# Kernel optimization log

Hardware: AMD Instinct MI355X
Metric: run time of the kernel (lower is better)

## Reference

```python
import jax, jax.numpy as jnp
import numpy as np

BLOCK_SIZE = 64
WINDOW_SIZE = 256  # local_window pattern: each query block attends to blocks within the window
NEG_INF = -1e30


def setup_inputs() -> dict:
    key = jax.random.key(0)
    kq, kk, kv = jax.random.split(key, 3)
    B, S, H, D = 2, 4096, 16, 64
    q = jax.random.normal(kq, (B, S, H, D), dtype=jnp.float32)
    k = jax.random.normal(kk, (B, S, H, D), dtype=jnp.float32)
    v = jax.random.normal(kv, (B, S, H, D), dtype=jnp.float32)
    return {"q": q, "k": k, "v": v}


def _block_sparse_attn(q, k, v):
    # q, k, v: [B, S, H, D]
    B, S, H, D = q.shape
    bs = BLOCK_SIZE
    N = S // bs                      # number of blocks
    W = WINDOW_SIZE // bs            # window in blocks (4)
    half = W // 2
    offsets = jnp.arange(-half, half + 1)          # [K] neighbor offsets, K = W+1 = 5
    K = offsets.shape[0]

    i = jnp.arange(N)
    j = i[:, None] + offsets[None, :]              # [N, K] neighbor block ids
    valid = (j >= 0) & (j < N)                     # boundary mask
    jc = jnp.clip(j, 0, N - 1)

    # reshape into blocks: [B, H, N, bs, D]
    qb = q.reshape(B, N, bs, H, D).transpose(0, 3, 1, 2, 4)
    kb = k.reshape(B, N, bs, H, D).transpose(0, 3, 1, 2, 4)
    vb = v.reshape(B, N, bs, H, D).transpose(0, 3, 1, 2, 4)

    # gather only the active (neighbor) key/value blocks: [B, H, N, K, bs, D]
    kn = kb[:, :, jc]
    vn = vb[:, :, jc]

    scale = 1.0 / jnp.sqrt(jnp.asarray(D, dtype=q.dtype))
    # block scores: [B, H, N, bs, K, bs]
    scores = jnp.einsum('bhnqd,bhnkcd->bhnqkc', qb, kn) * scale
    scores = jnp.where(valid[None, None, :, None, :, None], scores, NEG_INF)

    # softmax over the union of active key blocks for each query block
    scores = scores.reshape(B, H, N, bs, K * bs)
    attn = jax.nn.softmax(scores, axis=-1)
    out = jnp.einsum('bhnqe,bhned->bhnqd', attn, vn.reshape(B, H, N, K * bs, D))

    # back to [B, S, H, D]
    return out.transpose(0, 2, 3, 1, 4).reshape(B, S, H, D)


def reference(q, k, v):
    return _block_sparse_attn(q, k, v)
```

## Files before the change

### kernel.cpp

```cpp
#include <hip/hip_runtime.h>

#define S_DIM 4096
#define H_DIM 16
#define D_DIM 64
#define N_BLK 64
#define PITCH 72
#define NEG_INF_F (-1e30f)
#define QSCALE 0.125f

typedef __attribute__((ext_vector_type(4))) float f32x4;
typedef __attribute__((ext_vector_type(8))) short s16x8;
typedef __attribute__((ext_vector_type(4))) short s16x4;
typedef __attribute__((ext_vector_type(4))) unsigned int u32x4;
typedef __attribute__((ext_vector_type(2))) unsigned int u32x2;

__device__ __forceinline__ unsigned int fbits(float f) {
    return __builtin_bit_cast(unsigned int, f);
}
__device__ __forceinline__ unsigned int pkbf(float a, float b) {
    return __builtin_amdgcn_perm(fbits(b) + 0x8000u, fbits(a) + 0x8000u, 0x07060302u);
}
__device__ __forceinline__ short f2bf1(float f) {
    return (short)((fbits(f) + 0x8000u) >> 16);
}

__global__ __launch_bounds__(256, 4) void bsattn_kernel(
    const float* __restrict__ qg, const float* __restrict__ kg,
    const float* __restrict__ vg, float* __restrict__ outg)
{
    __shared__ short lds_k [N_BLK * PITCH];
    __shared__ short lds_vt[D_DIM * PITCH];

    const int tid  = threadIdx.x;
    const int w    = tid >> 6;
    const int lane = tid & 63;
    const int quad = lane >> 4;
    const int l16  = lane & 15;

    const int b  = blockIdx.z;
    const int h  = blockIdx.y;
    const int n0 = blockIdx.x << 1;
    const int n  = n0 + (w >> 1);
    const int qrow0 = n * 64 + (w & 1) * 32;

    s16x8 bq[2][2];
#pragma unroll
    for (int qt = 0; qt < 2; ++qt) {
        const size_t qrow = ((size_t)(b * S_DIM + qrow0 + qt * 16 + l16) * H_DIM + h) * D_DIM;
#pragma unroll
        for (int hh = 0; hh < 2; ++hh) {
            const float4* qp = reinterpret_cast<const float4*>(qg + qrow + hh * 32 + quad * 8);
            float4 f0 = qp[0];
            float4 f1 = qp[1];
            u32x4 u;
            u.x = pkbf(f0.x * QSCALE, f0.y * QSCALE);
            u.y = pkbf(f0.z * QSCALE, f0.w * QSCALE);
            u.z = pkbf(f1.x * QSCALE, f1.y * QSCALE);
            u.w = pkbf(f1.z * QSCALE, f1.w * QSCALE);
            bq[qt][hh] = __builtin_bit_cast(s16x8, u);
        }
    }

    f32x4 o[2][4];
    float m_run[2], l_run[2];
#pragma unroll
    for (int qt = 0; qt < 2; ++qt) {
        m_run[qt] = NEG_INF_F; l_run[qt] = 0.f;
#pragma unroll
        for (int dt = 0; dt < 4; ++dt) o[qt][dt] = (f32x4){0.f, 0.f, 0.f, 0.f};
    }

    const int tr = tid >> 2;
    const int d0 = (tid & 3) << 4;

    for (int ji = 0; ji < 6; ++ji) {
        const int j = n0 - 2 + ji;
        __syncthreads();
        if (j >= 0 && j < N_BLK) {
            const size_t src = ((size_t)(b * S_DIM + j * 64 + tr) * H_DIM + h) * D_DIM + d0;
            const float4* kp = reinterpret_cast<const float4*>(kg + src);
            const float4* vp = reinterpret_cast<const float4*>(vg + src);
            float4 k0 = kp[0], k1 = kp[1], k2 = kp[2], k3 = kp[3];
            float4 v0 = vp[0], v1 = vp[1], v2 = vp[2], v3 = vp[3];
            short* kd = lds_k + tr * PITCH + d0;
            u32x2 ka = {pkbf(k0.x, k0.y), pkbf(k0.z, k0.w)};
            u32x2 kb = {pkbf(k1.x, k1.y), pkbf(k1.z, k1.w)};
            u32x2 kc = {pkbf(k2.x, k2.y), pkbf(k2.z, k2.w)};
            u32x2 ke = {pkbf(k3.x, k3.y), pkbf(k3.z, k3.w)};
            *reinterpret_cast<u32x2*>(kd)      = ka;
            *reinterpret_cast<u32x2*>(kd + 4)  = kb;
            *reinterpret_cast<u32x2*>(kd + 8)  = kc;
            *reinterpret_cast<u32x2*>(kd + 12) = ke;
            float vf[16] = {v0.x, v0.y, v0.z, v0.w, v1.x, v1.y, v1.z, v1.w,
                            v2.x, v2.y, v2.z, v2.w, v3.x, v3.y, v3.z, v3.w};
#pragma unroll
            for (int i = 0; i < 16; ++i)
                lds_vt[(d0 + i) * PITCH + tr] = f2bf1(vf[i]);
        }
        __syncthreads();

        if (j < 0 || j >= N_BLK) continue;
        const int rel = j - n;
        if (rel < -2 || rel > 2) continue;

        f32x4 sa[2][4];
#pragma unroll
        for (int kt = 0; kt < 4; ++kt) {
            const short* kbp = lds_k + (kt * 16 + l16) * PITCH + quad * 8;
            s16x8 kf0 = *reinterpret_cast<const s16x8*>(kbp);
            s16x8 kf1 = *reinterpret_cast<const s16x8*>(kbp + 32);
            f32x4 z = {0.f, 0.f, 0.f, 0.f};
            f32x4 a0 = __builtin_amdgcn_mfma_f32_16x16x32_bf16(kf0, bq[0][0], z, 0, 0, 0);
            sa[0][kt] = __builtin_amdgcn_mfma_f32_16x16x32_bf16(kf1, bq[0][1], a0, 0, 0, 0);
            f32x4 a1 = __builtin_amdgcn_mfma_f32_16x16x32_bf16(kf0, bq[1][0], z, 0, 0, 0);
            sa[1][kt] = __builtin_amdgcn_mfma_f32_16x16x32_bf16(kf1, bq[1][1], a1, 0, 0, 0);
        }

        s16x8 pa[2][2];
#pragma unroll
        for (int qt = 0; qt < 2; ++qt) {
            float mx = NEG_INF_F;
#pragma unroll
            for (int kt = 0; kt < 4; ++kt)
#pragma unroll
                for (int r = 0; r < 4; ++r) mx = fmaxf(mx, sa[qt][kt][r]);
            mx = fmaxf(mx, __shfl_xor(mx, 16));
            mx = fmaxf(mx, __shfl_xor(mx, 32));
            const float mn = fmaxf(m_run[qt], mx);
            const float alpha = __expf(m_run[qt] - mn);
            m_run[qt] = mn;

            float rs = 0.f;
            unsigned int pk[4][2];
#pragma unroll
            for (int kt = 0; kt < 4; ++kt) {
                float e0 = __expf(sa[qt][kt][0] - mn);
                float e1 = __expf(sa[qt][kt][1] - mn);
                float e2 = __expf(sa[qt][kt][2] - mn);
                float e3 = __expf(sa[qt][kt][3] - mn);
                rs += (e0 + e1) + (e2 + e3);
                pk[kt][0] = pkbf(e0, e1);
                pk[kt][1] = pkbf(e2, e3);
            }
            rs += __shfl_xor(rs, 16);
            rs += __shfl_xor(rs, 32);
            l_run[qt] = l_run[qt] * alpha + rs;

            float ab[4];
#pragma unroll
            for (int r = 0; r < 4; ++r)
                ab[r] = __shfl(alpha, (lane & 48) + quad * 4 + r);
#pragma unroll
            for (int dt = 0; dt < 4; ++dt)
#pragma unroll
                for (int r = 0; r < 4; ++r) o[qt][dt][r] *= ab[r];

            pa[qt][0] = __builtin_bit_cast(s16x8, (u32x4){pk[0][0], pk[0][1], pk[1][0], pk[1][1]});
            pa[qt][1] = __builtin_bit_cast(s16x8, (u32x4){pk[2][0], pk[2][1], pk[3][0], pk[3][1]});
        }

#pragma unroll
        for (int dt = 0; dt < 4; ++dt) {
            const short* vb = lds_vt + (dt * 16 + l16) * PITCH + quad * 4;
            s16x4 v00 = *reinterpret_cast<const s16x4*>(vb);
            s16x4 v01 = *reinterpret_cast<const s16x4*>(vb + 16);
            s16x4 v10 = *reinterpret_cast<const s16x4*>(vb + 32);
            s16x4 v11 = *reinterpret_cast<const s16x4*>(vb + 48);
            s16x8 vf0 = {v00[0], v00[1], v00[2], v00[3], v01[0], v01[1], v01[2], v01[3]};
            s16x8 vf1 = {v10[0], v10[1], v10[2], v10[3], v11[0], v11[1], v11[2], v11[3]};
#pragma unroll
            for (int qt = 0; qt < 2; ++qt) {
                o[qt][dt] = __builtin_amdgcn_mfma_f32_16x16x32_bf16(pa[qt][0], vf0, o[qt][dt], 0, 0, 0);
                o[qt][dt] = __builtin_amdgcn_mfma_f32_16x16x32_bf16(pa[qt][1], vf1, o[qt][dt], 0, 0, 0);
            }
        }
    }

#pragma unroll
    for (int qt = 0; qt < 2; ++qt) {
#pragma unroll
        for (int r = 0; r < 4; ++r) {
            const float lb = __shfl(l_run[qt], (lane & 48) + quad * 4 + r);
            const float inv = 1.0f / lb;
            const int row = qrow0 + qt * 16 + quad * 4 + r;
            float* op = outg + ((size_t)(b * S_DIM + row) * H_DIM + h) * D_DIM + l16;
#pragma unroll
            for (int dt = 0; dt < 4; ++dt)
                op[dt * 16] = o[qt][dt][r] * inv;
        }
    }
}

extern "C" void kernel_launch(void* const* d_in, const int* in_sizes, int n_in,
                              void* d_out, int out_size, void* d_ws, size_t ws_size,
                              hipStream_t stream) {
    const float* q = (const float*)d_in[0];
    const float* k = (const float*)d_in[1];
    const float* v = (const float*)d_in[2];
    float* out = (float*)d_out;
    const int B = in_sizes[0] / (S_DIM * H_DIM * D_DIM);
    dim3 grid(N_BLK / 2, H_DIM, B);
    dim3 block(256);
    hipLaunchKernelGGL(bsattn_kernel, grid, block, 0, stream, q, k, v, out);
}
```

Baseline: 161.8 us.

## Double-buffer K/V tiles in LDS and prefetch next block into registers

Splits the K and transposed-V shared-memory tiles into two alternating buffers and issues the global loads for the next key block into registers before computing on the current one. This removes one barrier per iteration and lets global memory latency overlap with the MFMA and softmax work. In exchange it doubles LDS use (about 36 KB per block) and adds 32 live prefetch registers, which may reduce occupancy under the 4-blocks-per-CU launch bound.

After: 202.3 us. +25.0%, slower.

```diff
diff --git a/kernel.cpp b/kernel.cpp
--- a/kernel.cpp
+++ b/kernel.cpp
@@ -28,8 +28,8 @@
     const float* __restrict__ qg, const float* __restrict__ kg,
     const float* __restrict__ vg, float* __restrict__ outg)
 {
-    __shared__ short lds_k [N_BLK * PITCH];
-    __shared__ short lds_vt[D_DIM * PITCH];
+    __shared__ short lds_k [2 * N_BLK * PITCH];
+    __shared__ short lds_vt[2 * D_DIM * PITCH];
 
     const int tid  = threadIdx.x;
     const int w    = tid >> 6;
@@ -42,6 +42,22 @@
     const int n0 = blockIdx.x << 1;
     const int n  = n0 + (w >> 1);
     const int qrow0 = n * 64 + (w & 1) * 32;
+
+    const int tr = tid >> 2;
+    const int d0 = (tid & 3) << 4;
+    const size_t rowbase = ((size_t)(b * S_DIM + tr) * H_DIM + h) * D_DIM + d0;
+    const size_t jstride = (size_t)64 * H_DIM * D_DIM;
+
+    float4 pkf[4], pvf[4];
+    {
+        const int jn = n0 - 2;
+        if (jn >= 0) {
+            const float4* kp = reinterpret_cast<const float4*>(kg + rowbase + (size_t)jn * jstride);
+            const float4* vp = reinterpret_cast<const float4*>(vg + rowbase + (size_t)jn * jstride);
+            pkf[0] = kp[0]; pkf[1] = kp[1]; pkf[2] = kp[2]; pkf[3] = kp[3];
+            pvf[0] = vp[0]; pvf[1] = vp[1]; pvf[2] = vp[2]; pvf[3] = vp[3];
+        }
+    }
 
     s16x8 bq[2][2];
 #pragma unroll
@@ -70,108 +86,114 @@
         for (int dt = 0; dt < 4; ++dt) o[qt][dt] = (f32x4){0.f, 0.f, 0.f, 0.f};
     }
 
-    const int tr = tid >> 2;
-    const int d0 = (tid & 3) << 4;
-
     for (int ji = 0; ji < 6; ++ji) {
         const int j = n0 - 2 + ji;
-        __syncthreads();
+        const int bo = (ji & 1) * (N_BLK * PITCH);
+        short* const kbuf  = lds_k  + bo;
+        short* const vtbuf = lds_vt + bo;
+
         if (j >= 0 && j < N_BLK) {
-            const size_t src = ((size_t)(b * S_DIM + j * 64 + tr) * H_DIM + h) * D_DIM + d0;
-            const float4* kp = reinterpret_cast<const float4*>(kg + src);
-            const float4* vp = reinterpret_cast<const float4*>(vg + src);
-            float4 k0 = kp[0], k1 = kp[1], k2 = kp[2], k3 = kp[3];
-            float4 v0 = vp[0], v1 = vp[1], v2 = vp[2], v3 = vp[3];
-            short* kd = lds_k + tr * PITCH + d0;
-            u32x2 ka = {pkbf(k0.x, k0.y), pkbf(k0.z, k0.w)};
-            u32x2 kb = {pkbf(k1.x, k1.y), pkbf(k1.z, k1.w)};
-            u32x2 kc = {pkbf(k2.x, k2.y), pkbf(k2.z, k2.w)};
-            u32x2 ke = {pkbf(k3.x, k3.y), pkbf(k3.z, k3.w)};
+            short* kd = kbuf + tr * PITCH + d0;
+            u32x2 ka = {pkbf(pkf[0].x, pkf[0].y), pkbf(pkf[0].z, pkf[0].w)};
+            u32x2 kb = {pkbf(pkf[1].x, pkf[1].y), pkbf(pkf[1].z, pkf[1].w)};
+            u32x2 kc = {pkbf(pkf[2].x, pkf[2].y), pkbf(pkf[2].z, pkf[2].w)};
+            u32x2 ke = {pkbf(pkf[3].x, pkf[3].y), pkbf(pkf[3].z, pkf[3].w)};
             *reinterpret_cast<u32x2*>(kd)      = ka;
             *reinterpret_cast<u32x2*>(kd + 4)  = kb;
             *reinterpret_cast<u32x2*>(kd + 8)  = kc;
             *reinterpret_cast<u32x2*>(kd + 12) = ke;
-            float vf[16] = {v0.x, v0.y, v0.z, v0.w, v1.x, v1.y, v1.z, v1.w,
-                            v2.x, v2.y, v2.z, v2.w, v3.x, v3.y, v3.z, v3.w};
+            float vf[16] = {pvf[0].x, pvf[0].y, pvf[0].z, pvf[0].w,
+                            pvf[1].x, pvf[1].y, pvf[1].z, pvf[1].w,
+                            pvf[2].x, pvf[2].y, pvf[2].z, pvf[2].w,
+                            pvf[3].x, pvf[3].y, pvf[3].z, pvf[3].w};
 #pragma unroll
             for (int i = 0; i < 16; ++i)
-                lds_vt[(d0 + i) * PITCH + tr] = f2bf1(vf[i]);
+                vtbuf[(d0 + i) * PITCH + tr] = f2bf1(vf[i]);
         }
         __syncthreads();
 
-        if (j < 0 || j >= N_BLK) continue;
+        if (ji < 5) {
+            const int jn = j + 1;
+            if (jn >= 0 && jn < N_BLK) {
+                const float4* kp = reinterpret_cast<const float4*>(kg + rowbase + (size_t)jn * jstride);
+                const float4* vp = reinterpret_cast<const float4*>(vg + rowbase + (size_t)jn * jstride);
+                pkf[0] = kp[0]; pkf[1] = kp[1]; pkf[2] = kp[2]; pkf[3] = kp[3];
+                pvf[0] = vp[0]; pvf[1] = vp[1]; pvf[2] = vp[2]; pvf[3] = vp[3];
+            }
+        }
+
         const int rel = j - n;
-        if (rel < -2 || rel > 2) continue;
-
-        f32x4 sa[2][4];
-#pragma unroll
-        for (int kt = 0; kt < 4; ++kt) {
-            const short* kbp = lds_k + (kt * 16 + l16) * PITCH + quad * 8;
-            s16x8 kf0 = *reinterpret_cast<const s16x8*>(kbp);
-            s16x8 kf1 = *reinterpret_cast<const s16x8*>(kbp + 32);
-            f32x4 z = {0.f, 0.f, 0.f, 0.f};
-            f32x4 a0 = __builtin_amdgcn_mfma_f32_16x16x32_bf16(kf0, bq[0][0], z, 0, 0, 0);
-            sa[0][kt] = __builtin_amdgcn_mfma_f32_16x16x32_bf16(kf1, bq[0][1], a0, 0, 0, 0);
-            f32x4 a1 = __builtin_amdgcn_mfma_f32_16x16x32_bf16(kf0, bq[1][0], z, 0, 0, 0);
-            sa[1][kt] = __builtin_amdgcn_mfma_f32_16x16x32_bf16(kf1, bq[1][1], a1, 0, 0, 0);
-        }
-
-        s16x8 pa[2][2];
-#pragma unroll
-        for (int qt = 0; qt < 2; ++qt) {
-            float mx = NEG_INF_F;
-#pragma unroll
-            for (int kt = 0; kt < 4; ++kt)
-#pragma unroll
-                for (int r = 0; r < 4; ++r) mx = fmaxf(mx, sa[qt][kt][r]);
-            mx = fmaxf(mx, __shfl_xor(mx, 16));
-            mx = fmaxf(mx, __shfl_xor(mx, 32));
-            const float mn = fmaxf(m_run[qt], mx);
-            const float alpha = __expf(m_run[qt] - mn);
-            m_run[qt] = mn;
-
-            float rs = 0.f;
-            unsigned int pk[4][2];
+        if (j >= 0 && j < N_BLK && rel >= -2 && rel <= 2) {
+            f32x4 sa[2][4];
 #pragma unroll
             for (int kt = 0; kt < 4; ++kt) {
-                float e0 = __expf(sa[qt][kt][0] - mn);
-                float e1 = __expf(sa[qt][kt][1] - mn);
-                float e2 = __expf(sa[qt][kt][2] - mn);
-                float e3 = __expf(sa[qt][kt][3] - mn);
-                rs += (e0 + e1) + (e2 + e3);
-                pk[kt][0] = pkbf(e0, e1);
-                pk[kt][1] = pkbf(e2, e3);
-            }
-            rs += __shfl_xor(rs, 16);
-            rs += __shfl_xor(rs, 32);
-            l_run[qt] = l_run[qt] * alpha + rs;
-
-            float ab[4];
-#pragma unroll
-            for (int r = 0; r < 4; ++r)
-                ab[r] = __shfl(alpha, (lane & 48) + quad * 4 + r);
-#pragma unroll
-            for (int dt = 0; dt < 4; ++dt)
-#pragma unroll
-                for (int r = 0; r < 4; ++r) o[qt][dt][r] *= ab[r];
-
-            pa[qt][0] = __builtin_bit_cast(s16x8, (u32x4){pk[0][0], pk[0][1], pk[1][0], pk[1][1]});
-            pa[qt][1] = __builtin_bit_cast(s16x8, (u32x4){pk[2][0], pk[2][1], pk[3][0], pk[3][1]});
-        }
-
-#pragma unroll
-        for (int dt = 0; dt < 4; ++dt) {
-            const short* vb = lds_vt + (dt * 16 + l16) * PITCH + quad * 4;
-            s16x4 v00 = *reinterpret_cast<const s16x4*>(vb);
-            s16x4 v01 = *reinterpret_cast<const s16x4*>(vb + 16);
-            s16x4 v10 = *reinterpret_cast<const s16x4*>(vb + 32);
-            s16x4 v11 = *reinterpret_cast<const s16x4*>(vb + 48);
-            s16x8 vf0 = {v00[0], v00[1], v00[2], v00[3], v01[0], v01[1], v01[2], v01[3]};
-            s16x8 vf1 = {v10[0], v10[1], v10[2], v10[3], v11[0], v11[1], v11[2], v11[3]};
+                const short* kbp = kbuf + (kt * 16 + l16) * PITCH + quad * 8;
+                s16x8 kf0 = *reinterpret_cast<const s16x8*>(kbp);
+                s16x8 kf1 = *reinterpret_cast<const s16x8*>(kbp + 32);
+                f32x4 z = {0.f, 0.f, 0.f, 0.f};
+                f32x4 a0 = __builtin_amdgcn_mfma_f32_16x16x32_bf16(kf0, bq[0][0], z, 0, 0, 0);
+                sa[0][kt] = __builtin_amdgcn_mfma_f32_16x16x32_bf16(kf1, bq[0][1], a0, 0, 0, 0);
+                f32x4 a1 = __builtin_amdgcn_mfma_f32_16x16x32_bf16(kf0, bq[1][0], z, 0, 0, 0);
+                sa[1][kt] = __builtin_amdgcn_mfma_f32_16x16x32_bf16(kf1, bq[1][1], a1, 0, 0, 0);
+            }
+
+            s16x8 pa[2][2];
 #pragma unroll
             for (int qt = 0; qt < 2; ++qt) {
-                o[qt][dt] = __builtin_amdgcn_mfma_f32_16x16x32_bf16(pa[qt][0], vf0, o[qt][dt], 0, 0, 0);
-                o[qt][dt] = __builtin_amdgcn_mfma_f32_16x16x32_bf16(pa[qt][1], vf1, o[qt][dt], 0, 0, 0);
+                float mx = NEG_INF_F;
+#pragma unroll
+                for (int kt = 0; kt < 4; ++kt)
+#pragma unroll
+                    for (int r = 0; r < 4; ++r) mx = fmaxf(mx, sa[qt][kt][r]);
+                mx = fmaxf(mx, __shfl_xor(mx, 16));
+                mx = fmaxf(mx, __shfl_xor(mx, 32));
+                const float mn = fmaxf(m_run[qt], mx);
+                const float alpha = __expf(m_run[qt] - mn);
+                m_run[qt] = mn;
+
+                float rs = 0.f;
+                unsigned int pk[4][2];
+#pragma unroll
+                for (int kt = 0; kt < 4; ++kt) {
+                    float e0 = __expf(sa[qt][kt][0] - mn);
+                    float e1 = __expf(sa[qt][kt][1] - mn);
+                    float e2 = __expf(sa[qt][kt][2] - mn);
+                    float e3 = __expf(sa[qt][kt][3] - mn);
+                    rs += (e0 + e1) + (e2 + e3);
+                    pk[kt][0] = pkbf(e0, e1);
+                    pk[kt][1] = pkbf(e2, e3);
+                }
+                rs += __shfl_xor(rs, 16);
+                rs += __shfl_xor(rs, 32);
+                l_run[qt] = l_run[qt] * alpha + rs;
+
+                float ab[4];
+#pragma unroll
+                for (int r = 0; r < 4; ++r)
+                    ab[r] = __shfl(alpha, (lane & 48) + quad * 4 + r);
+#pragma unroll
+                for (int dt = 0; dt < 4; ++dt)
+#pragma unroll
+                    for (int r = 0; r < 4; ++r) o[qt][dt][r] *= ab[r];
+
+                pa[qt][0] = __builtin_bit_cast(s16x8, (u32x4){pk[0][0], pk[0][1], pk[1][0], pk[1][1]});
+                pa[qt][1] = __builtin_bit_cast(s16x8, (u32x4){pk[2][0], pk[2][1], pk[3][0], pk[3][1]});
+            }
+
+#pragma unroll
+            for (int dt = 0; dt < 4; ++dt) {
+                const short* vb = vtbuf + (dt * 16 + l16) * PITCH + quad * 4;
+                s16x4 v00 = *reinterpret_cast<const s16x4*>(vb);
+                s16x4 v01 = *reinterpret_cast<const s16x4*>(vb + 16);
+                s16x4 v10 = *reinterpret_cast<const s16x4*>(vb + 32);
+                s16x4 v11 = *reinterpret_cast<const s16x4*>(vb + 48);
+                s16x8 vf0 = {v00[0], v00[1], v00[2], v00[3], v01[0], v01[1], v01[2], v01[3]};
+                s16x8 vf1 = {v10[0], v10[1], v10[2], v10[3], v11[0], v11[1], v11[2], v11[3]};
+#pragma unroll
+                for (int qt = 0; qt < 2; ++qt) {
+                    o[qt][dt] = __builtin_amdgcn_mfma_f32_16x16x32_bf16(pa[qt][0], vf0, o[qt][dt], 0, 0, 0);
+                    o[qt][dt] = __builtin_amdgcn_mfma_f32_16x16x32_bf16(pa[qt][1], vf1, o[qt][dt], 0, 0, 0);
+                }
             }
         }
     }
```

## Give each wave a full query block, stage all V once, read K from global

Applied to the files above, without the earlier changes.

Each workgroup now covers four query blocks, one per wave. The union of eight V blocks is loaded into LDS once, transposed into packed bf16 pairs with a rotating swizzle, and followed by a single barrier. K fragments are loaded directly from global memory into registers per wave, which removes the per-iteration K staging and the pair of barriers per key block. The grid halves and the register footprint grows (launch bounds drop to 2 waves per SIMD). K reads are duplicated across waves and rely on cache, and LDS use grows to 64KB.

Result: no change. 160.6 us (-0.8%).

```diff
diff --git a/kernel.cpp b/kernel.cpp
--- a/kernel.cpp
+++ b/kernel.cpp
@@ -4,13 +4,11 @@
 #define H_DIM 16
 #define D_DIM 64
 #define N_BLK 64
-#define PITCH 72
 #define NEG_INF_F (-1e30f)
 #define QSCALE 0.125f
 
 typedef __attribute__((ext_vector_type(4))) float f32x4;
 typedef __attribute__((ext_vector_type(8))) short s16x8;
-typedef __attribute__((ext_vector_type(4))) short s16x4;
 typedef __attribute__((ext_vector_type(4))) unsigned int u32x4;
 typedef __attribute__((ext_vector_type(2))) unsigned int u32x2;
 
@@ -20,16 +18,12 @@
 __device__ __forceinline__ unsigned int pkbf(float a, float b) {
     return __builtin_amdgcn_perm(fbits(b) + 0x8000u, fbits(a) + 0x8000u, 0x07060302u);
 }
-__device__ __forceinline__ short f2bf1(float f) {
-    return (short)((fbits(f) + 0x8000u) >> 16);
-}
-
-__global__ __launch_bounds__(256, 4) void bsattn_kernel(
+
+__global__ __launch_bounds__(256, 2) void bsattn_kernel(
     const float* __restrict__ qg, const float* __restrict__ kg,
     const float* __restrict__ vg, float* __restrict__ outg)
 {
-    __shared__ short lds_k [N_BLK * PITCH];
-    __shared__ short lds_vt[D_DIM * PITCH];
+    __shared__ unsigned int lds_vt[D_DIM * 256];
 
     const int tid  = threadIdx.x;
     const int w    = tid >> 6;
@@ -39,14 +33,13 @@
 
     const int b  = blockIdx.z;
     const int h  = blockIdx.y;
-    const int n0 = blockIdx.x << 1;
-    const int n  = n0 + (w >> 1);
-    const int qrow0 = n * 64 + (w & 1) * 32;
-
-    s16x8 bq[2][2];
-#pragma unroll
-    for (int qt = 0; qt < 2; ++qt) {
-        const size_t qrow = ((size_t)(b * S_DIM + qrow0 + qt * 16 + l16) * H_DIM + h) * D_DIM;
+    const int n0 = blockIdx.x << 2;
+    const int n  = n0 + w;
+
+    s16x8 bq[4][2];
+#pragma unroll
+    for (int qt = 0; qt < 4; ++qt) {
+        const size_t qrow = ((size_t)(b * S_DIM + n * 64 + qt * 16 + l16) * H_DIM + h) * D_DIM;
 #pragma unroll
         for (int hh = 0; hh < 2; ++hh) {
             const float4* qp = reinterpret_cast<const float4*>(qg + qrow + hh * 32 + quad * 8);
@@ -61,69 +54,91 @@
         }
     }
 
-    f32x4 o[2][4];
-    float m_run[2], l_run[2];
-#pragma unroll
-    for (int qt = 0; qt < 2; ++qt) {
+    {
+        const int jt = tid >> 5;
+        const int sp = tid & 31;
+        const int jv = n0 - 2 + jt;
+        if (jv >= 0 && jv < N_BLK) {
+            const float* v0p = vg + ((size_t)(b * S_DIM + jv * 64 + 2 * sp) * H_DIM + h) * D_DIM;
+            const float* v1p = v0p + H_DIM * D_DIM;
+            const int craw = jt * 64 + 2 * sp;
+#pragma unroll
+            for (int ch = 0; ch < 4; ++ch) {
+                const int d0 = ch * 16;
+                const float4* ap = reinterpret_cast<const float4*>(v0p + d0);
+                const float4* bp = reinterpret_cast<const float4*>(v1p + d0);
+                float4 a0 = ap[0], a1 = ap[1], a2 = ap[2], a3 = ap[3];
+                float4 b0 = bp[0], b1 = bp[1], b2 = bp[2], b3 = bp[3];
+                float av[16] = {a0.x,a0.y,a0.z,a0.w, a1.x,a1.y,a1.z,a1.w,
+                                a2.x,a2.y,a2.z,a2.w, a3.x,a3.y,a3.z,a3.w};
+                float bv[16] = {b0.x,b0.y,b0.z,b0.w, b1.x,b1.y,b1.z,b1.w,
+                                b2.x,b2.y,b2.z,b2.w, b3.x,b3.y,b3.z,b3.w};
+#pragma unroll
+                for (int i = 0; i < 16; ++i) {
+                    const int d = d0 + i;
+                    lds_vt[d * 256 + (((craw + 8 * d) & 511) >> 1)] = pkbf(av[i], bv[i]);
+                }
+            }
+        }
+    }
+
+    f32x4 o[4][4];
+    float m_run[4], l_run[4];
+#pragma unroll
+    for (int qt = 0; qt < 4; ++qt) {
         m_run[qt] = NEG_INF_F; l_run[qt] = 0.f;
 #pragma unroll
         for (int dt = 0; dt < 4; ++dt) o[qt][dt] = (f32x4){0.f, 0.f, 0.f, 0.f};
     }
 
-    const int tr = tid >> 2;
-    const int d0 = (tid & 3) << 4;
-
-    for (int ji = 0; ji < 6; ++ji) {
-        const int j = n0 - 2 + ji;
-        __syncthreads();
-        if (j >= 0 && j < N_BLK) {
-            const size_t src = ((size_t)(b * S_DIM + j * 64 + tr) * H_DIM + h) * D_DIM + d0;
-            const float4* kp = reinterpret_cast<const float4*>(kg + src);
-            const float4* vp = reinterpret_cast<const float4*>(vg + src);
-            float4 k0 = kp[0], k1 = kp[1], k2 = kp[2], k3 = kp[3];
-            float4 v0 = vp[0], v1 = vp[1], v2 = vp[2], v3 = vp[3];
-            short* kd = lds_k + tr * PITCH + d0;
-            u32x2 ka = {pkbf(k0.x, k0.y), pkbf(k0.z, k0.w)};
-            u32x2 kb = {pkbf(k1.x, k1.y), pkbf(k1.z, k1.w)};
-            u32x2 kc = {pkbf(k2.x, k2.y), pkbf(k2.z, k2.w)};
-            u32x2 ke = {pkbf(k3.x, k3.y), pkbf(k3.z, k3.w)};
-            *reinterpret_cast<u32x2*>(kd)      = ka;
-            *reinterpret_cast<u32x2*>(kd + 4)  = kb;
-            *reinterpret_cast<u32x2*>(kd + 8)  = kc;
-            *reinterpret_cast<u32x2*>(kd + 12) = ke;
-            float vf[16] = {v0.x, v0.y, v0.z, v0.w, v1.x, v1.y, v1.z, v1.w,
-                            v2.x, v2.y, v2.z, v2.w, v3.x, v3.y, v3.z, v3.w};
-#pragma unroll
-            for (int i = 0; i < 16; ++i)
-                lds_vt[(d0 + i) * PITCH + tr] = f2bf1(vf[i]);
-        }
-        __syncthreads();
-
+    __syncthreads();
+
+    const int colb = quad * 4 + 8 * l16;
+
+    for (int t = 0; t < 5; ++t) {
+        const int j = n - 2 + t;
         if (j < 0 || j >= N_BLK) continue;
-        const int rel = j - n;
-        if (rel < -2 || rel > 2) continue;
-
-        f32x4 sa[2][4];
+        const int ji = w + t;
+
+        float4 kf[4][2][2];
 #pragma unroll
         for (int kt = 0; kt < 4; ++kt) {
-            const short* kbp = lds_k + (kt * 16 + l16) * PITCH + quad * 8;
-            s16x8 kf0 = *reinterpret_cast<const s16x8*>(kbp);
-            s16x8 kf1 = *reinterpret_cast<const s16x8*>(kbp + 32);
-            f32x4 z = {0.f, 0.f, 0.f, 0.f};
-            f32x4 a0 = __builtin_amdgcn_mfma_f32_16x16x32_bf16(kf0, bq[0][0], z, 0, 0, 0);
-            sa[0][kt] = __builtin_amdgcn_mfma_f32_16x16x32_bf16(kf1, bq[0][1], a0, 0, 0, 0);
-            f32x4 a1 = __builtin_amdgcn_mfma_f32_16x16x32_bf16(kf0, bq[1][0], z, 0, 0, 0);
-            sa[1][kt] = __builtin_amdgcn_mfma_f32_16x16x32_bf16(kf1, bq[1][1], a1, 0, 0, 0);
-        }
-
-        s16x8 pa[2][2];
-#pragma unroll
-        for (int qt = 0; qt < 2; ++qt) {
+            const size_t krow = ((size_t)(b * S_DIM + j * 64 + kt * 16 + l16) * H_DIM + h) * D_DIM + quad * 8;
+#pragma unroll
+            for (int hh = 0; hh < 2; ++hh) {
+                const float4* kp = reinterpret_cast<const float4*>(kg + krow + hh * 32);
+                kf[kt][hh][0] = kp[0];
+                kf[kt][hh][1] = kp[1];
+            }
+        }
+        s16x8 kbf[4][2];
+#pragma unroll
+        for (int kt = 0; kt < 4; ++kt)
+#pragma unroll
+            for (int hh = 0; hh < 2; ++hh) {
+                u32x4 u;
+                u.x = pkbf(kf[kt][hh][0].x, kf[kt][hh][0].y);
+                u.y = pkbf(kf[kt][hh][0].z, kf[kt][hh][0].w);
+                u.z = pkbf(kf[kt][hh][1].x, kf[kt][hh][1].y);
+                u.w = pkbf(kf[kt][hh][1].z, kf[kt][hh][1].w);
+                kbf[kt][hh] = __builtin_bit_cast(s16x8, u);
+            }
+
+        s16x8 pa[4][2];
+#pragma unroll
+        for (int qt = 0; qt < 4; ++qt) {
+            f32x4 sa[4];
+#pragma unroll
+            for (int kt = 0; kt < 4; ++kt) {
+                f32x4 z = {0.f, 0.f, 0.f, 0.f};
+                f32x4 a0 = __builtin_amdgcn_mfma_f32_16x16x32_bf16(kbf[kt][0], bq[qt][0], z, 0, 0, 0);
+                sa[kt]   = __builtin_amdgcn_mfma_f32_16x16x32_bf16(kbf[kt][1], bq[qt][1], a0, 0, 0, 0);
+            }
             float mx = NEG_INF_F;
 #pragma unroll
             for (int kt = 0; kt < 4; ++kt)
 #pragma unroll
-                for (int r = 0; r < 4; ++r) mx = fmaxf(mx, sa[qt][kt][r]);
+                for (int r = 0; r < 4; ++r) mx = fmaxf(mx, sa[kt][r]);
             mx = fmaxf(mx, __shfl_xor(mx, 16));
             mx = fmaxf(mx, __shfl_xor(mx, 32));
             const float mn = fmaxf(m_run[qt], mx);
@@ -134,10 +149,10 @@
             unsigned int pk[4][2];
 #pragma unroll
             for (int kt = 0; kt < 4; ++kt) {
-                float e0 = __expf(sa[qt][kt][0] - mn);
-                float e1 = __expf(sa[qt][kt][1] - mn);
-                float e2 = __expf(sa[qt][kt][2] - mn);
-                float e3 = __expf(sa[qt][kt][3] - mn);
+                float e0 = __expf(sa[kt][0] - mn);
+                float e1 = __expf(sa[kt][1] - mn);
+                float e2 = __expf(sa[kt][2] - mn);
+                float e3 = __expf(sa[kt][3] - mn);
                 rs += (e0 + e1) + (e2 + e3);
                 pk[kt][0] = pkbf(e0, e1);
                 pk[kt][1] = pkbf(e2, e3);
@@ -159,17 +174,20 @@
             pa[qt][1] = __builtin_bit_cast(s16x8, (u32x4){pk[2][0], pk[2][1], pk[3][0], pk[3][1]});
         }
 
+        const int cb0 = ji * 64 + colb;
 #pragma unroll
         for (int dt = 0; dt < 4; ++dt) {
-            const short* vb = lds_vt + (dt * 16 + l16) * PITCH + quad * 4;
-            s16x4 v00 = *reinterpret_cast<const s16x4*>(vb);
-            s16x4 v01 = *reinterpret_cast<const s16x4*>(vb + 16);
-            s16x4 v10 = *reinterpret_cast<const s16x4*>(vb + 32);
-            s16x4 v11 = *reinterpret_cast<const s16x4*>(vb + 48);
-            s16x8 vf0 = {v00[0], v00[1], v00[2], v00[3], v01[0], v01[1], v01[2], v01[3]};
-            s16x8 vf1 = {v10[0], v10[1], v10[2], v10[3], v11[0], v11[1], v11[2], v11[3]};
-#pragma unroll
-            for (int qt = 0; qt < 2; ++qt) {
+            const int d = dt * 16 + l16;
+            const unsigned int* vrow = lds_vt + d * 256;
+            const int cb = cb0 + 128 * dt;
+            u32x2 v00 = *reinterpret_cast<const u32x2*>(vrow + (((cb     ) & 511) >> 1));
+            u32x2 v01 = *reinterpret_cast<const u32x2*>(vrow + (((cb + 16) & 511) >> 1));
+            u32x2 v10 = *reinterpret_cast<const u32x2*>(vrow + (((cb + 32) & 511) >> 1));
+            u32x2 v11 = *reinterpret_cast<const u32x2*>(vrow + (((cb + 48) & 511) >> 1));
+            s16x8 vf0 = __builtin_bit_cast(s16x8, (u32x4){v00.x, v00.y, v01.x, v01.y});
+            s16x8 vf1 = __builtin_bit_cast(s16x8, (u32x4){v10.x, v10.y, v11.x, v11.y});
+#pragma unroll
+            for (int qt = 0; qt < 4; ++qt) {
                 o[qt][dt] = __builtin_amdgcn_mfma_f32_16x16x32_bf16(pa[qt][0], vf0, o[qt][dt], 0, 0, 0);
                 o[qt][dt] = __builtin_amdgcn_mfma_f32_16x16x32_bf16(pa[qt][1], vf1, o[qt][dt], 0, 0, 0);
             }
@@ -177,12 +195,12 @@
     }
 
 #pragma unroll
-    for (int qt = 0; qt < 2; ++qt) {
+    for (int qt = 0; qt < 4; ++qt) {
 #pragma unroll
         for (int r = 0; r < 4; ++r) {
             const float lb = __shfl(l_run[qt], (lane & 48) + quad * 4 + r);
             const float inv = 1.0f / lb;
-            const int row = qrow0 + qt * 16 + quad * 4 + r;
+            const int row = n * 64 + qt * 16 + quad * 4 + r;
             float* op = outg + ((size_t)(b * S_DIM + row) * H_DIM + h) * D_DIM + l16;
 #pragma unroll
             for (int dt = 0; dt < 4; ++dt)
@@ -199,7 +217,7 @@
     const float* v = (const float*)d_in[2];
     float* out = (float*)d_out;
     const int B = in_sizes[0] / (S_DIM * H_DIM * D_DIM);
-    dim3 grid(N_BLK / 2, H_DIM, B);
+    dim3 grid(N_BLK / 4, H_DIM, B);
     dim3 block(256);
     hipLaunchKernelGGL(bsattn_kernel, grid, block, 0, stream, q, k, v, out);
 }
```
